# Optimization experiments

Measured on AMD Instinct MI355X. Metric: run time of the kernel, lower is better.

The kernel has to match this reference:

```python
import jax, jax.numpy as jnp
import numpy as np

EPS = 1e-8

def setup_inputs() -> dict:
    key = jax.random.key(0)
    k1, k2 = jax.random.split(key)
    B, C, H, W = 8, 21, 512, 512
    inp = jax.random.normal(k1, (B, C, H, W), dtype=jnp.float32)
    target = jax.random.uniform(k2, (B, C, H, W), dtype=jnp.float32)
    return {"input": inp, "target": target}

def reference(input, target):
    B, C, H, W = input.shape
    # argmax over class dim -> [B, H, W]
    pred = jnp.argmax(input, axis=1)
    # one-hot of prediction, flattened over spatial dims -> [B, HW, C]
    h = jax.nn.one_hot(pred.reshape(B, H * W), C, dtype=input.dtype)
    # target flattened over spatial dims -> [B, C, HW]
    y = target.reshape(B, C, H * W)
    # cm[b, i, j] = sum_n y[b, i, n] * h[b, n, j]  -> [B, C, C]
    cm = jnp.einsum('bin,bnj->bij', y, h)
    # row-normalize by target mass per class, then mean over batch -> [C, C]
    cm = cm / (jnp.sum(y, axis=2, keepdims=True) + EPS)
    return jnp.mean(cm, axis=0)
```

## Files before the change

kernel.cpp:

```cpp
#include <hip/hip_runtime.h>

#define NC 21
#define NB 8
#define HW (512*512)
#define EPS 1e-8f

__global__ __launch_bounds__(256) void cm_accum(const float* __restrict__ input,
                                                const float* __restrict__ target,
                                                float* __restrict__ cm ) {
    __shared__ float scm[NC * NC];
    const int t = threadIdx.x;
    for (int i = t; i < NC * NC; i += 256) scm[i] = 0.0f;
    __syncthreads();

    const int b    = blockIdx.x >> 8;
    const int tile = blockIdx.x & 255;
    const int q    = (tile << 8) + t;

    const float4* ip = (const float4*)(input  + (size_t)b * NC * HW);
    const float4* tp = (const float4*)(target + (size_t)b * NC * HW);
    const int plane4 = HW / 4;

    float4 m = ip[q];
    int jx = 0, jy = 0, jz = 0, jw = 0;
    #pragma unroll
    for (int c = 1; c < NC; ++c) {
        float4 v = ip[c * plane4 + q];
        if (v.x > m.x) { m.x = v.x; jx = c; }
        if (v.y > m.y) { m.y = v.y; jy = c; }
        if (v.z > m.z) { m.z = v.z; jz = c; }
        if (v.w > m.w) { m.w = v.w; jw = c; }
    }

    #pragma unroll
    for (int i = 0; i < NC; ++i) {
        float4 y = tp[i * plane4 + q];
        const int row = i * NC;
        atomicAdd(&scm[row + jx], y.x);
        atomicAdd(&scm[row + jy], y.y);
        atomicAdd(&scm[row + jz], y.z);
        atomicAdd(&scm[row + jw], y.w);
    }
    __syncthreads();

    for (int i = t; i < NC * NC; i += 256) atomicAdd(&cm[b * NC * NC + i], scm[i]);
}

__global__ __launch_bounds__(512) void cm_final(const float* __restrict__ cm,
                                                float* __restrict__ out) {
    __shared__ float rs[NB * NC];
    const int t = threadIdx.x;
    if (t < NB * NC) {
        const int b = t / NC, i = t % NC;
        float s = 0.0f;
        for (int j = 0; j < NC; ++j) s += cm[b * NC * NC + i * NC + j];
        rs[t] = s + EPS;
    }
    __syncthreads();
    if (t < NC * NC) {
        const int i = t / NC;
        float acc = 0.0f;
        for (int b = 0; b < NB; ++b) acc += cm[b * NC * NC + t] / rs[b * NC + i];
        out[t] = acc * (1.0f / NB);
    }
}

extern "C" void kernel_launch(void* const* d_in, const int* in_sizes, int n_in,
                              void* d_out, int out_size, void* d_ws, size_t ws_size,
                              hipStream_t stream) {
    const float* input  = (const float*)d_in[0];
    const float* target = (const float*)d_in[1];
    float* out = (float*)d_out;
    float* cm  = (float*)d_ws;

    hipMemsetAsync(cm, 0, NB * NC * NC * sizeof(float), stream);
    cm_accum<<<NB * 256, 256, 0, stream>>>(input, target, cm);
    cm_final<<<1, 512, 0, stream>>>(cm, out);
}
```

Baseline: 494.0 us.

## Replace global atomics with per-block partials, batch loads, add reduce kernel

Each accumulation block now writes its shared-memory confusion matrix to its own slot in a partial buffer instead of doing global atomicAdds. A new reduce kernel sums those partials per batch in segments. All 21 input planes are loaded before the argmax, and target planes are fetched in groups of 7, to raise memory-level parallelism. The change adds a kernel launch and a partial-buffer round trip, uses more registers, and falls back to 8 tiles per block when the workspace is too small.

```diff
diff --git a/kernel.cpp b/kernel.cpp
--- a/kernel.cpp
+++ b/kernel.cpp
@@ -4,46 +4,80 @@
 #define NB 8
 #define HW (512*512)
 #define EPS 1e-8f
+#define CM_N (NC * NC)
 
 __global__ __launch_bounds__(256) void cm_accum(const float* __restrict__ input,
                                                 const float* __restrict__ target,
-                                                float* __restrict__ cm ) {
-    __shared__ float scm[NC * NC];
+                                                float* __restrict__ partial,
+                                                int tilesPerBlock) {
+    __shared__ float scm[CM_N];
     const int t = threadIdx.x;
-    for (int i = t; i < NC * NC; i += 256) scm[i] = 0.0f;
+    for (int i = t; i < CM_N; i += 256) scm[i] = 0.0f;
     __syncthreads();
 
-    const int b    = blockIdx.x >> 8;
-    const int tile = blockIdx.x & 255;
-    const int q    = (tile << 8) + t;
+    const int tilesPerBatch  = 256;
+    const int blocksPerBatch = tilesPerBatch / tilesPerBlock;
+    const int b     = blockIdx.x / blocksPerBatch;
+    const int tile0 = (blockIdx.x % blocksPerBatch) * tilesPerBlock;
 
     const float4* ip = (const float4*)(input  + (size_t)b * NC * HW);
     const float4* tp = (const float4*)(target + (size_t)b * NC * HW);
     const int plane4 = HW / 4;
 
-    float4 m = ip[q];
-    int jx = 0, jy = 0, jz = 0, jw = 0;
-    #pragma unroll
-    for (int c = 1; c < NC; ++c) {
-        float4 v = ip[c * plane4 + q];
-        if (v.x > m.x) { m.x = v.x; jx = c; }
-        if (v.y > m.y) { m.y = v.y; jy = c; }
-        if (v.z > m.z) { m.z = v.z; jz = c; }
-        if (v.w > m.w) { m.w = v.w; jw = c; }
-    }
+    for (int tt = 0; tt < tilesPerBlock; ++tt) {
+        const int q = (tile0 + tt) * 256 + t;
 
-    #pragma unroll
-    for (int i = 0; i < NC; ++i) {
-        float4 y = tp[i * plane4 + q];
-        const int row = i * NC;
-        atomicAdd(&scm[row + jx], y.x);
-        atomicAdd(&scm[row + jy], y.y);
-        atomicAdd(&scm[row + jz], y.z);
-        atomicAdd(&scm[row + jw], y.w);
+        float4 v[NC];
+        #pragma unroll
+        for (int c = 0; c < NC; ++c) v[c] = ip[c * plane4 + q];
+
+        float4 m = v[0];
+        int jx = 0, jy = 0, jz = 0, jw = 0;
+        #pragma unroll
+        for (int c = 1; c < NC; ++c) {
+            if (v[c].x > m.x) { m.x = v[c].x; jx = c; }
+            if (v[c].y > m.y) { m.y = v[c].y; jy = c; }
+            if (v[c].z > m.z) { m.z = v[c].z; jz = c; }
+            if (v[c].w > m.w) { m.w = v[c].w; jw = c; }
+        }
+
+        #pragma unroll
+        for (int i0 = 0; i0 < NC; i0 += 7) {
+            float4 y[7];
+            #pragma unroll
+            for (int k = 0; k < 7; ++k) y[k] = tp[(i0 + k) * plane4 + q];
+            #pragma unroll
+            for (int k = 0; k < 7; ++k) {
+                const int row = (i0 + k) * NC;
+                atomicAdd(&scm[row + jx], y[k].x);
+                atomicAdd(&scm[row + jy], y[k].y);
+                atomicAdd(&scm[row + jz], y[k].z);
+                atomicAdd(&scm[row + jw], y[k].w);
+            }
+        }
     }
     __syncthreads();
 
-    for (int i = t; i < NC * NC; i += 256) atomicAdd(&cm[b * NC * NC + i], scm[i]);
+    float* dst = partial + (size_t)blockIdx.x * CM_N;
+    for (int i = t; i < CM_N; i += 256) dst[i] = scm[i];
+}
+
+__global__ __launch_bounds__(256) void cm_reduce(const float* __restrict__ partial,
+                                                 float* __restrict__ cm,
+                                                 int blocksPerBatch, int segs) {
+    const int b   = blockIdx.x / segs;
+    const int s   = blockIdx.x % segs;
+    const int per = blocksPerBatch / segs;
+    const float* base = partial + ((size_t)b * blocksPerBatch + (size_t)s * per) * CM_N;
+    const int t = threadIdx.x;
+    float a0 = 0.0f, a1 = 0.0f;
+    for (int k = 0; k < per; ++k) {
+        const float* p = base + (size_t)k * CM_N;
+        a0 += p[t];
+        if (t < CM_N - 256) a1 += p[256 + t];
+    }
+    atomicAdd(&cm[b * CM_N + t], a0);
+    if (t < CM_N - 256) atomicAdd(&cm[b * CM_N + 256 + t], a1);
 }
 
 __global__ __launch_bounds__(512) void cm_final(const float* __restrict__ cm,
@@ -53,14 +87,14 @@
     if (t < NB * NC) {
         const int b = t / NC, i = t % NC;
         float s = 0.0f;
-        for (int j = 0; j < NC; ++j) s += cm[b * NC * NC + i * NC + j];
+        for (int j = 0; j < NC; ++j) s += cm[b * CM_N + i * NC + j];
         rs[t] = s + EPS;
     }
     __syncthreads();
-    if (t < NC * NC) {
+    if (t < CM_N) {
         const int i = t / NC;
         float acc = 0.0f;
-        for (int b = 0; b < NB; ++b) acc += cm[b * NC * NC + t] / rs[b * NC + i];
+        for (int b = 0; b < NB; ++b) acc += cm[b * CM_N + t] / rs[b * NC + i];
         out[t] = acc * (1.0f / NB);
     }
 }
@@ -71,9 +105,19 @@
     const float* input  = (const float*)d_in[0];
     const float* target = (const float*)d_in[1];
     float* out = (float*)d_out;
-    float* cm  = (float*)d_ws;
 
-    hipMemsetAsync(cm, 0, NB * NC * NC * sizeof(float), stream);
-    cm_accum<<<NB * 256, 256, 0, stream>>>(input, target, cm);
+    float* cm      = (float*)d_ws;
+    float* partial = cm + NB * CM_N;
+
+    int T = 1;
+    size_t need = ((size_t)NB * 256 / T * CM_N + NB * CM_N) * sizeof(float);
+    if (ws_size < need) T = 8;
+    const int blocksPerBatch = 256 / T;
+    const int numBlocks = NB * blocksPerBatch;
+    const int segs = blocksPerBatch >= 8 ? 8 : 1;
+
+    hipMemsetAsync(cm, 0, NB * CM_N * sizeof(float), stream);
+    cm_accum<<<numBlocks, 256, 0, stream>>>(input, target, partial, T);
+    cm_reduce<<<NB * segs, 256, 0, stream>>>(partial, cm, blocksPerBatch, segs);
     cm_final<<<1, 512, 0, stream>>>(cm, out);
 }
```

Measured after the change: 501.9 us. About the same (+1.6%).

## Split argmax and scatter into separate kernels with per-wave shared tables

Applied to the files above, without the earlier changes.

Splits the fused kernel into three. An argmax kernel uses two interleaved max chains and writes byte predictions to workspace. A scatter kernel gives each wave its own shared-memory table to cut LDS atomic contention, processes four pixel groups per block, and writes per-block partials. A reduce kernel sums the partials with fewer global atomics. In exchange it adds a pred round trip through memory and two extra launches.

```diff
diff --git a/kernel.cpp b/kernel.cpp
--- a/kernel.cpp
+++ b/kernel.cpp
@@ -4,46 +4,91 @@
 #define NB 8
 #define HW (512*512)
 #define EPS 1e-8f
+#define CM_N (NC * NC)
+#define PLANE4 (HW / 4)
 
-__global__ __launch_bounds__(256) void cm_accum(const float* __restrict__ input,
-                                                const float* __restrict__ target,
-                                                float* __restrict__ cm ) {
-    __shared__ float scm[NC * NC];
+__global__ __launch_bounds__(256) void k_argmax(const float* __restrict__ input,
+                                                uchar4* __restrict__ pred4) {
+    const int g = blockIdx.x * 256 + threadIdx.x;
+    const int b = g >> 16;
+    const int q = g & 65535;
+    const float4* ip = (const float4*)(input + (size_t)b * NC * HW);
+
+    float4 m0 = ip[q];
+    float4 m1 = ip[PLANE4 + q];
+    int j0x = 0, j0y = 0, j0z = 0, j0w = 0;
+    int j1x = 1, j1y = 1, j1z = 1, j1w = 1;
+    #pragma unroll
+    for (int c = 2; c < NC; c += 2) {
+        float4 v0 = ip[c * PLANE4 + q];
+        float4 v1 = (c + 1 < NC) ? ip[(c + 1) * PLANE4 + q] : make_float4(0, 0, 0, 0);
+        if (v0.x > m0.x) { m0.x = v0.x; j0x = c; }
+        if (v0.y > m0.y) { m0.y = v0.y; j0y = c; }
+        if (v0.z > m0.z) { m0.z = v0.z; j0z = c; }
+        if (v0.w > m0.w) { m0.w = v0.w; j0w = c; }
+        if (c + 1 < NC) {
+            if (v1.x > m1.x) { m1.x = v1.x; j1x = c + 1; }
+            if (v1.y > m1.y) { m1.y = v1.y; j1y = c + 1; }
+            if (v1.z > m1.z) { m1.z = v1.z; j1z = c + 1; }
+            if (v1.w > m1.w) { m1.w = v1.w; j1w = c + 1; }
+        }
+    }
+    int jx = (m1.x > m0.x || (m1.x == m0.x && j1x < j0x)) ? j1x : j0x;
+    int jy = (m1.y > m0.y || (m1.y == m0.y && j1y < j0y)) ? j1y : j0y;
+    int jz = (m1.z > m0.z || (m1.z == m0.z && j1z < j0z)) ? j1z : j0z;
+    int jw = (m1.w > m0.w || (m1.w == m0.w && j1w < j0w)) ? j1w : j0w;
+    pred4[g] = make_uchar4((unsigned char)jx, (unsigned char)jy,
+                           (unsigned char)jz, (unsigned char)jw);
+}
+
+__global__ __launch_bounds__(256) void k_scatter(const float* __restrict__ target,
+                                                 const uchar4* __restrict__ pred4,
+                                                 float* __restrict__ partial) {
+    __shared__ float tbl[4 * CM_N];
     const int t = threadIdx.x;
-    for (int i = t; i < NC * NC; i += 256) scm[i] = 0.0f;
+    for (int i = t; i < 4 * CM_N; i += 256) tbl[i] = 0.0f;
     __syncthreads();
+    float* wt = tbl + (t >> 6) * CM_N;
 
-    const int b    = blockIdx.x >> 8;
-    const int tile = blockIdx.x & 255;
-    const int q    = (tile << 8) + t;
+    const int b  = blockIdx.x >> 6;
+    const int q0 = (blockIdx.x & 63) * 1024;
+    const float4* tp = (const float4*)(target + (size_t)b * NC * HW);
+    const uchar4* pp = pred4 + (size_t)b * PLANE4;
 
-    const float4* ip = (const float4*)(input  + (size_t)b * NC * HW);
-    const float4* tp = (const float4*)(target + (size_t)b * NC * HW);
-    const int plane4 = HW / 4;
-
-    float4 m = ip[q];
-    int jx = 0, jy = 0, jz = 0, jw = 0;
-    #pragma unroll
-    for (int c = 1; c < NC; ++c) {
-        float4 v = ip[c * plane4 + q];
-        if (v.x > m.x) { m.x = v.x; jx = c; }
-        if (v.y > m.y) { m.y = v.y; jy = c; }
-        if (v.z > m.z) { m.z = v.z; jz = c; }
-        if (v.w > m.w) { m.w = v.w; jw = c; }
-    }
-
-    #pragma unroll
-    for (int i = 0; i < NC; ++i) {
-        float4 y = tp[i * plane4 + q];
-        const int row = i * NC;
-        atomicAdd(&scm[row + jx], y.x);
-        atomicAdd(&scm[row + jy], y.y);
-        atomicAdd(&scm[row + jz], y.z);
-        atomicAdd(&scm[row + jw], y.w);
+    for (int it = 0; it < 4; ++it) {
+        const int q = q0 + it * 256 + t;
+        const uchar4 pj = pp[q];
+        #pragma unroll
+        for (int i = 0; i < NC; ++i) {
+            float4 y = tp[i * PLANE4 + q];
+            const int row = i * NC;
+            atomicAdd(&wt[row + pj.x], y.x);
+            atomicAdd(&wt[row + pj.y], y.y);
+            atomicAdd(&wt[row + pj.z], y.z);
+            atomicAdd(&wt[row + pj.w], y.w);
+        }
     }
     __syncthreads();
 
-    for (int i = t; i < NC * NC; i += 256) atomicAdd(&cm[b * NC * NC + i], scm[i]);
+    float* dst = partial + (size_t)blockIdx.x * CM_N;
+    for (int i = t; i < CM_N; i += 256)
+        dst[i] = tbl[i] + tbl[CM_N + i] + tbl[2 * CM_N + i] + tbl[3 * CM_N + i];
+}
+
+__global__ __launch_bounds__(256) void cm_reduce(const float* __restrict__ partial,
+                                                 float* __restrict__ cm) {
+    const int b = blockIdx.x >> 3;
+    const int s = blockIdx.x & 7;
+    const float* base = partial + ((size_t)b * 64 + (size_t)s * 8) * CM_N;
+    const int t = threadIdx.x;
+    float a0 = 0.0f, a1 = 0.0f;
+    for (int k = 0; k < 8; ++k) {
+        const float* p = base + (size_t)k * CM_N;
+        a0 += p[t];
+        if (t < CM_N - 256) a1 += p[256 + t];
+    }
+    atomicAdd(&cm[b * CM_N + t], a0);
+    if (t < CM_N - 256) atomicAdd(&cm[b * CM_N + 256 + t], a1);
 }
 
 __global__ __launch_bounds__(512) void cm_final(const float* __restrict__ cm,
@@ -53,14 +98,14 @@
     if (t < NB * NC) {
         const int b = t / NC, i = t % NC;
         float s = 0.0f;
-        for (int j = 0; j < NC; ++j) s += cm[b * NC * NC + i * NC + j];
+        for (int j = 0; j < NC; ++j) s += cm[b * CM_N + i * NC + j];
         rs[t] = s + EPS;
     }
     __syncthreads();
-    if (t < NC * NC) {
+    if (t < CM_N) {
         const int i = t / NC;
         float acc = 0.0f;
-        for (int b = 0; b < NB; ++b) acc += cm[b * NC * NC + t] / rs[b * NC + i];
+        for (int b = 0; b < NB; ++b) acc += cm[b * CM_N + t] / rs[b * NC + i];
         out[t] = acc * (1.0f / NB);
     }
 }
@@ -71,9 +116,14 @@
     const float* input  = (const float*)d_in[0];
     const float* target = (const float*)d_in[1];
     float* out = (float*)d_out;
-    float* cm  = (float*)d_ws;
 
-    hipMemsetAsync(cm, 0, NB * NC * NC * sizeof(float), stream);
-    cm_accum<<<NB * 256, 256, 0, stream>>>(input, target, cm);
-    cm_final<<<1, 512, 0, stream>>>(cm, out);
+    float*  cm      = (float*)d_ws;
+    float*  partial = cm + NB * CM_N;
+    uchar4* pred4   = (uchar4*)(partial + 512 * CM_N);
+
+    hipMemsetAsync(cm, 0, NB * CM_N * sizeof(float), stream);
+    k_argmax <<<NB * 256, 256, 0, stream>>>(input, pred4);
+    k_scatter<<<512,      256, 0, stream>>>(target, pred4, partial);
+    cm_reduce<<<64,       256, 0, stream>>>(partial, cm);
+    cm_final <<<1,        512, 0, stream>>>(cm, out);
 }
```

Measured after the change: 525.4 us. +6.4%, slower.
